# Kernel tuning notes

Measured on AMD Instinct MI355X. Metric: run time of the kernel, lower is better.

Reference implementation:

```python
import jax, jax.numpy as jnp
import numpy as np

DT = 0.01
EPS = 1e-5


def setup_inputs() -> dict:
    key = jax.random.key(0)
    ks = jax.random.split(key, 20)
    B, H, IN, COV, CH, OH, OUT = 1024, 64, 8, 16, 64, 128, 2
    NE, OPE = 400, 256            # events, observations per event
    TOT = NE * OPE

    def w(k, sh, sc=0.05):
        return jax.random.normal(k, sh, dtype=jnp.float32) * sc

    return {
        'time_uniq': jnp.arange(NE, dtype=jnp.float32) * DT,   # event k fires at grid step k
        'time_ptr': jnp.arange(NE + 1, dtype=jnp.int32) * OPE,  # uniform obs per event
        'X': jax.random.normal(ks[0], (TOT, IN), dtype=jnp.float32),
        'sample_ids': jax.random.randint(ks[1], (TOT,), 0, B, dtype=jnp.int32),
        'covs': jax.random.normal(ks[2], (B, COV), dtype=jnp.float32),
        'T': 5,
        'cov_W1': w(ks[3], (CH, COV)), 'cov_b1': jnp.zeros((CH,), jnp.float32),
        'cov_W2': w(ks[4], (H, CH)),   'cov_b2': jnp.zeros((H,), jnp.float32),
        'gb_Wih': w(ks[5], (3 * H, IN)), 'gb_Whh': w(ks[6], (3 * H, H)),
        'gb_bih': jnp.zeros((3 * H,), jnp.float32), 'gb_bhh': jnp.zeros((3 * H,), jnp.float32),
        'gx_W': w(ks[7], (3 * H, 1)), 'gx_b': jnp.zeros((3 * H,), jnp.float32),
        'ghr_W': w(ks[8], (H, H)), 'ghz_W': w(ks[9], (H, H)), 'ghh_W': w(ks[10], (H, H)),
        'out_W1': w(ks[11], (OH, H)), 'out_b1': jnp.zeros((OH,), jnp.float32),
        'out_W2': w(ks[12], (OUT, OH)), 'out_b2': jnp.zeros((OUT,), jnp.float32),
    }


def _forward(time_uniq, time_ptr, X, sample_ids, covs, T,
             cov_W1, cov_b1, cov_W2, cov_b2,
             gb_Wih, gb_Whh, gb_bih, gb_bhh,
             gx_W, gx_b, ghr_W, ghz_W, ghh_W,
             out_W1, out_b1, out_W2, out_b2):
    n_events = time_uniq.shape[0]
    ope = X.shape[0] // n_events          # uniform observations per event (static)
    n_steps = int(round(T / DT))
    delta_t = DT

    # covariates_map (dropout p=0 -> identity)
    h0 = jnp.tanh(jnp.maximum(covs @ cov_W1.T + cov_b1, 0.0) @ cov_W2.T + cov_b2)

    def gru_bayes(x, h):                  # torch.nn.GRUCell semantics (gates r,z,n)
        gi = x @ gb_Wih.T + gb_bih
        gh = h @ gb_Whh.T + gb_bhh
        ir, iz, inn = jnp.split(gi, 3, axis=1)
        hr, hz, hn = jnp.split(gh, 3, axis=1)
        r = jax.nn.sigmoid(ir + hr)
        z = jax.nn.sigmoid(iz + hz)
        n = jnp.tanh(inn + r * hn)
        return (1.0 - z) * n + z * h

    def gru_ode(h):                       # FullGRUODECell with x = zeros
        px = jnp.zeros((h.shape[0], 1), h.dtype)
        gx = px @ gx_W.T + gx_b
        xr, xz, xh = jnp.split(gx, 3, axis=1)
        r = jax.nn.sigmoid(xr + h @ ghr_W.T)
        z = jax.nn.sigmoid(xz + h @ ghz_W.T)
        u = jnp.tanh(xh + (r * h) @ ghh_W.T)
        return h + delta_t * (1.0 - z) * (u - h)

    times = jnp.arange(n_steps, dtype=jnp.float32) * DT
    offs = jnp.arange(ope)

    def step(carry, t):
        h, i = carry
        ic = jnp.minimum(i, n_events - 1)
        fire = (i < n_events) & (time_uniq[ic] <= t + EPS)   # <=1 event per grid step
        obs = time_ptr[ic] + offs
        idx = sample_ids[obs]
        h_upd = h.at[idx].set(gru_bayes(X[obs], h[idx]))
        h = jnp.where(fire, h_upd, h)
        i = i + fire.astype(i.dtype)
        h_rec = h                          # recorded after events, before ODE step
        h = gru_ode(h)
        return (h, i), h_rec

    (h_last, _), h_steps = jax.lax.scan(step, (h0, jnp.int32(0)), times)
    h_path = jnp.concatenate([h_steps, h_last[None]], axis=0)   # [n_steps+1, B, H]

    # net_out (dropout p=0 -> identity)
    o = jnp.maximum(jnp.einsum('tbh,oh->tbo', h_path, out_W1) + out_b1, 0.0)
    return jnp.einsum('tbh,oh->tbo', o, out_W2) + out_b2


def reference(time_uniq, time_ptr, X, sample_ids, covs, T,
              cov_W1, cov_b1, cov_W2, cov_b2,
              gb_Wih, gb_Whh, gb_bih, gb_bhh,
              gx_W, gx_b, ghr_W, ghz_W, ghh_W,
              out_W1, out_b1, out_W2, out_b2):
    return _forward(time_uniq, time_ptr, X, sample_ids, covs, T,
                    cov_W1, cov_b1, cov_W2, cov_b2,
                    gb_Wih, gb_Whh, gb_bih, gb_bhh,
                    gx_W, gx_b, ghr_W, ghz_W, ghh_W,
                    out_W1, out_b1, out_W2, out_b2)
```

## Files before the change

### kernel.cpp

```cpp
#include <hip/hip_runtime.h>

#define DT_F 0.01f
#define EPS_F 1e-5f
#define NEG_INF_I (-1073741824)

typedef _Float16 f16;
typedef _Float16 f16x2 __attribute__((ext_vector_type(2)));
typedef _Float16 f16x8 __attribute__((ext_vector_type(8)));
typedef float f32x4 __attribute__((ext_vector_type(4)));

#define MFMA16(a, b, c) __builtin_amdgcn_mfma_f32_16x16x32_f16((a), (b), (c), 0, 0, 0)

__device__ __forceinline__ float rl(float v, int l) {
  return __int_as_float(__builtin_amdgcn_readlane(__float_as_int(v), l));
}
__device__ __forceinline__ float sigm(float x) {
  float e = __builtin_amdgcn_exp2f(-1.442695041f * x);
  return __builtin_amdgcn_rcpf(1.0f + e);
}
__device__ __forceinline__ float tanhf_fast(float x) {
  float e = __builtin_amdgcn_exp2f(2.885390082f * x);
  return fmaf(-2.0f, __builtin_amdgcn_rcpf(e + 1.0f), 1.0f);
}
__device__ __forceinline__ float dot2(unsigned w, unsigned h, float acc) {
  return __builtin_amdgcn_fdot2(__builtin_bit_cast(f16x2, w),
                                __builtin_bit_cast(f16x2, h), acc, false);
}
__device__ __forceinline__ unsigned packf16(float a, float b) {
  return __builtin_bit_cast(unsigned, __builtin_amdgcn_cvt_pkrtz(a, b));
}
#define PINQ(v) asm volatile("" : "+v"((v).x), "+v"((v).y), "+v"((v).z), "+v"((v).w))

__global__ void build_evtab_kernel(const int* __restrict__ sample_ids,
                                   const int* __restrict__ time_ptr,
                                   int* __restrict__ evtab, int B, int ope) {
  int k = blockIdx.x;
  int base = time_ptr[k];
  for (int t = threadIdx.x; t < ope; t += blockDim.x) {
    int obs = base + t;
    int sid = sample_ids[obs];
    atomicMax(&evtab[k * B + sid], obs + 1);
  }
}

__global__ void pack_pairs_kernel(const float* __restrict__ ghr,
                                  const float* __restrict__ ghz,
                                  const float* __restrict__ ghh,
                                  const float* __restrict__ gbWhh,
                                  const float* __restrict__ gbWih,
                                  unsigned* __restrict__ odeP,
                                  unsigned* __restrict__ bayP,
                                  unsigned* __restrict__ wihP, int IN) {
  int idx = blockIdx.x * 256 + threadIdx.x;
  if (idx < 3 * 64 * 32) {
    int p = idx & 31, r = idx >> 5;
    int g = r >> 6, i = r & 63;
    const float* src = (g == 0) ? ghr : ((g == 1) ? ghz : ghh);
    odeP[idx] = packf16(src[i * 64 + 2 * p], src[i * 64 + 2 * p + 1]);
    bayP[idx] = packf16(gbWhh[r * 64 + 2 * p], gbWhh[r * 64 + 2 * p + 1]);
  }
  if (idx < 3 * 64 * 4) {
    int p = idx & 3, r = idx >> 2;
    float a = (2 * p < IN) ? gbWih[r * IN + 2 * p] : 0.0f;
    float b = (2 * p + 1 < IN) ? gbWih[r * IN + 2 * p + 1] : 0.0f;
    wihP[idx] = packf16(a, b);
  }
}

__global__ void pack_head_kernel(const float* __restrict__ W1, f16* __restrict__ w1P) {
  int f = blockIdx.x;
  int l = threadIdx.x;
  int t = f >> 1, kf = f & 1;
  int n = 16 * t + (l & 15);
  for (int j = 0; j < 8; ++j) {
    int k = 8 * (l >> 4) + j + 32 * kf;
    w1P[f * 512 + l * 8 + j] = (f16)W1[n * 64 + k];
  }
}

__global__ __launch_bounds__(256, 1) void evolve_kernel(
    const float* __restrict__ time_uniq,
    const float* __restrict__ X,
    const float* __restrict__ covs,
    const float* __restrict__ cov_W1, const float* __restrict__ cov_b1,
    const float* __restrict__ cov_W2, const float* __restrict__ cov_b2,
    const float* __restrict__ gb_bih, const float* __restrict__ gb_bhh,
    const float* __restrict__ gx_b,
    const unsigned* __restrict__ odeP, const unsigned* __restrict__ bayP,
    const unsigned* __restrict__ wihP,
    const int* __restrict__ evtab,
    f16* __restrict__ hp16,
    int B, int NE, int n_steps, int IN, int COV)
{
  __shared__ unsigned sBW[3 * 64 * 32];
  __shared__ int sStep[1024];
  __shared__ __align__(16) f16 sH16[4][64];
  __shared__ __align__(16) f16 sRH16[4][64];

  const int tid = threadIdx.x;
  const int wid = tid >> 6, lane = tid & 63;
  const int b = blockIdx.x * 4 + wid;
  const bool alive = (b < B);

  for (int idx = tid; idx < 3 * 64 * 32; idx += 256) {
    int c = idx & 31, r = idx >> 5;
    int i = r & 63, s = c >> 2;
    sBW[r * 32 + (((s ^ (i & 7)) << 2) | (c & 3))] = bayP[idx];
  }
  if (wid == 0) {
    int pm = NEG_INF_I;
    int loc[16];
#pragma unroll
    for (int j = 0; j < 16; ++j) {
      int e = lane * 16 + j;
      int gv = NEG_INF_I;
      if (e < NE && e < 1024) {
        float tu = time_uniq[e];
        int k0 = (int)floorf((tu - EPS_F) * 100.0f) - 2;
        if (k0 < 0) k0 = 0;
        while ((float)k0 * DT_F + EPS_F < tu) ++k0;
        gv = k0 - e;
      }
      pm = max(pm, gv);
      loc[j] = pm;
    }
    int tot = pm;
#pragma unroll
    for (int off = 1; off < 64; off <<= 1) {
      int v = __shfl_up(tot, off);
      if (lane >= off) tot = max(tot, v);
    }
    int excl = __shfl_up(tot, 1);
    if (lane == 0) excl = NEG_INF_I;
#pragma unroll
    for (int j = 0; j < 16; ++j)
      sStep[lane * 16 + j] = lane * 16 + j + max(loc[j], excl);
  }
  __syncthreads();

  const uint4* odeQ = (const uint4*)odeP;
  uint4 WR[8], WZ[8], WU[8];
#pragma unroll
  for (int q = 0; q < 8; ++q) {
    WR[q] = odeQ[(0 * 64 + lane) * 8 + q];
    WZ[q] = odeQ[(1 * 64 + lane) * 8 + q];
    WU[q] = odeQ[(2 * 64 + lane) * 8 + q];
  }
  const uint4* wihQ = (const uint4*)wihP;

  const float xr = gx_b[lane], xz = gx_b[64 + lane], xh = gx_b[128 + lane];
  const float crz_r = gb_bih[lane] + gb_bhh[lane];
  const float crz_z = gb_bih[64 + lane] + gb_bhh[64 + lane];
  const float bihn = gb_bih[128 + lane], bhhn = gb_bhh[128 + lane];

  float h = 0.0f;
  if (alive) {
    float cacc = cov_b1[lane];
    for (int c = 0; c < COV; ++c)
      cacc = fmaf(covs[b * COV + c], cov_W1[lane * COV + c], cacc);
    float cl = fmaxf(cacc, 0.0f);
    float hacc = cov_b2[lane];
#pragma unroll
    for (int j = 0; j < 64; ++j)
      hacc = fmaf(rl(cl, j), cov_W2[lane * 64 + j], hacc);
    h = tanhf_fast(hacc);
  }
  sH16[wid][lane] = (f16)h;

  int e_next = 0, s_next = 0x7fffffff, v_cur = 0, v_pipe = 0;
  float xf[8];
#pragma unroll
  for (int kk = 0; kk < 8; ++kk) xf[kk] = 0.0f;
  if (alive && NE > 0) {
    s_next = sStep[0];
    v_cur = evtab[b];
    if (v_cur > 0) {
      const float* xp = X + (long)(v_cur - 1) * IN;
#pragma unroll
      for (int kk = 0; kk < 8; ++kk) xf[kk] = (kk < IN) ? xp[kk] : 0.0f;
    }
    v_pipe = (NE > 1) ? evtab[B + b] : 0;
  } else if (NE > 0) {
    s_next = sStep[0];
  }

  const uint4* hq4 = (const uint4*)sH16[wid];
  const uint4* rq4 = (const uint4*)sRH16[wid];
  f16* hps = hp16 + (long)b * 64 + lane;
  const long rowstride = (long)B * 64;

  uint4 hpre[8];
#pragma unroll
  for (int q = 0; q < 8; ++q) hpre[q] = hq4[q];

#pragma unroll 1
  for (int k = 0; k < n_steps; ++k) {
#pragma unroll
    for (int q = 0; q < 8; ++q) { PINQ(WR[q]); PINQ(WZ[q]); PINQ(WU[q]); }

    if (k == s_next) {
      if (v_cur > 0) {
        unsigned xp0 = packf16(xf[0], xf[1]), xp1 = packf16(xf[2], xf[3]);
        unsigned xp2 = packf16(xf[4], xf[5]), xp3 = packf16(xf[6], xf[7]);
        uint4 wxr = wihQ[lane], wxz = wihQ[64 + lane], wxn = wihQ[128 + lane];
        float ar = crz_r, az = crz_z, anh = bhhn, ani = bihn;
        ar = dot2(wxr.x, xp0, ar); ar = dot2(wxr.y, xp1, ar);
        ar = dot2(wxr.z, xp2, ar); ar = dot2(wxr.w, xp3, ar);
        az = dot2(wxz.x, xp0, az); az = dot2(wxz.y, xp1, az);
        az = dot2(wxz.z, xp2, az); az = dot2(wxz.w, xp3, az);
        ani = dot2(wxn.x, xp0, ani); ani = dot2(wxn.y, xp1, ani);
        ani = dot2(wxn.z, xp2, ani); ani = dot2(wxn.w, xp3, ani);
        float ar1 = 0.f, az1 = 0.f, an1 = 0.f;
#pragma unroll
        for (int q = 0; q < 8; ++q) {
          uint4 hh = hpre[q];
          int sw = ((q ^ (lane & 7)) << 2);
          uint4 br = *(const uint4*)&sBW[(0 * 64 + lane) * 32 + sw];
          uint4 bz = *(const uint4*)&sBW[(1 * 64 + lane) * 32 + sw];
          uint4 bn = *(const uint4*)&sBW[(2 * 64 + lane) * 32 + sw];
          ar  = dot2(br.x, hh.x, ar);   ar1 = dot2(br.y, hh.y, ar1);
          ar  = dot2(br.z, hh.z, ar);   ar1 = dot2(br.w, hh.w, ar1);
          az  = dot2(bz.x, hh.x, az);   az1 = dot2(bz.y, hh.y, az1);
          az  = dot2(bz.z, hh.z, az);   az1 = dot2(bz.w, hh.w, az1);
          anh = dot2(bn.x, hh.x, anh);  an1 = dot2(bn.y, hh.y, an1);
          anh = dot2(bn.z, hh.z, anh);  an1 = dot2(bn.w, hh.w, an1);
        }
        float r = sigm(ar + ar1);
        float z = sigm(az + az1);
        float n = tanhf_fast(ani + r * (anh + an1));
        h = (1.0f - z) * n + z * h;
        sH16[wid][lane] = (f16)h;
#pragma unroll
        for (int q = 0; q < 8; ++q) hpre[q] = hq4[q];
      }
      ++e_next;
      if (e_next < NE && e_next < 1024) {
        s_next = sStep[e_next];
        v_cur = v_pipe;
        if (v_cur > 0) {
          const float* xp = X + (long)(v_cur - 1) * IN;
#pragma unroll
          for (int kk = 0; kk < 8; ++kk) xf[kk] = (kk < IN) ? xp[kk] : 0.0f;
        }
        v_pipe = (e_next + 1 < NE) ? evtab[(long)(e_next + 1) * B + b] : 0;
      } else {
        s_next = 0x7fffffff;
        v_cur = 0;
      }
    }

    if (alive)
      hps[(long)k * rowstride] = (f16)h;

    float ar0 = xr, ar1 = 0.f, ar2 = 0.f, ar3 = 0.f;
    float az0 = xz, az1 = 0.f, az2 = 0.f, az3 = 0.f;
#pragma unroll
    for (int q = 0; q < 8; ++q) {
      uint4 hp = hpre[q];
      ar0 = dot2(WR[q].x, hp.x, ar0); ar1 = dot2(WR[q].y, hp.y, ar1);
      ar2 = dot2(WR[q].z, hp.z, ar2); ar3 = dot2(WR[q].w, hp.w, ar3);
      az0 = dot2(WZ[q].x, hp.x, az0); az1 = dot2(WZ[q].y, hp.y, az1);
      az2 = dot2(WZ[q].z, hp.z, az2); az3 = dot2(WZ[q].w, hp.w, az3);
    }
    float r = sigm((ar0 + ar1) + (ar2 + ar3));
    float z = sigm((az0 + az1) + (az2 + az3));
    sRH16[wid][lane] = (f16)(r * h);

    float au0 = xh, au1 = 0.f, au2 = 0.f, au3 = 0.f;
#pragma unroll
    for (int q = 0; q < 8; ++q) {
      uint4 rp = rq4[q];
      au0 = dot2(WU[q].x, rp.x, au0); au1 = dot2(WU[q].y, rp.y, au1);
      au2 = dot2(WU[q].z, rp.z, au2); au3 = dot2(WU[q].w, rp.w, au3);
    }
    float u = tanhf_fast((au0 + au1) + (au2 + au3));
    h = fmaf(DT_F * (1.0f - z), u - h, h);
    sH16[wid][lane] = (f16)h;
#pragma unroll
    for (int q = 0; q < 8; ++q) hpre[q] = hq4[q];
  }

  if (alive)
    hps[(long)n_steps * rowstride] = (f16)h;
}

__global__ __launch_bounds__(256, 4) void head_mfma_kernel(
    const f16* __restrict__ hp16, const f16* __restrict__ w1P,
    const float* __restrict__ b1, const float* __restrict__ W2,
    const float* __restrict__ b2, float* __restrict__ out, long nrows)
{
  const int wq = threadIdx.x >> 6, lane = threadIdx.x & 63;
  const int col = lane & 15;
  const long rowbase = ((long)blockIdx.x * 4 + wq) * 64;

  f16x8 Wf[8][2];
#pragma unroll
  for (int t = 0; t < 8; ++t)
#pragma unroll
    for (int kf = 0; kf < 2; ++kf)
      Wf[t][kf] = ((const f16x8*)w1P)[(2 * t + kf) * 64 + lane];

  float b1v[8], w2a[8], w2b[8];
#pragma unroll
  for (int t = 0; t < 8; ++t) {
    b1v[t] = b1[16 * t + col];
    w2a[t] = W2[16 * t + col];
    w2b[t] = W2[128 + 16 * t + col];
  }
  const float b20 = b2[0], b21 = b2[1];

#pragma unroll 1
  for (int g = 0; g < 4; ++g) {
    long row0 = rowbase + g * 16;
    long arow = row0 + col;
    f16x8 aH0 = {0, 0, 0, 0, 0, 0, 0, 0}, aH1 = aH0;
    if (arow < nrows) {
      const f16x8* ap = (const f16x8*)(hp16 + arow * 64);
      aH0 = ap[lane >> 4];
      aH1 = ap[(lane >> 4) + 4];
    }
    float p0[4] = {0.f, 0.f, 0.f, 0.f}, p1[4] = {0.f, 0.f, 0.f, 0.f};
#pragma unroll
    for (int t = 0; t < 8; ++t) {
      f32x4 c = {0.f, 0.f, 0.f, 0.f};
      c = MFMA16(aH0, Wf[t][0], c);
      c = MFMA16(aH1, Wf[t][1], c);
#pragma unroll
      for (int i = 0; i < 4; ++i) {
        float o = fmaxf(c[i] + b1v[t], 0.0f);
        p0[i] = fmaf(o, w2a[t], p0[i]);
        p1[i] = fmaf(o, w2b[t], p1[i]);
      }
    }
#pragma unroll
    for (int off = 1; off < 16; off <<= 1) {
#pragma unroll
      for (int i = 0; i < 4; ++i) {
        p0[i] += __shfl_xor(p0[i], off);
        p1[i] += __shfl_xor(p1[i], off);
      }
    }
    if (col == 0) {
#pragma unroll
      for (int i = 0; i < 4; ++i) {
        long row = row0 + (lane >> 4) * 4 + i;
        if (row < nrows) {
          out[row * 2 + 0] = p0[i] + b20;
          out[row * 2 + 1] = p1[i] + b21;
        }
      }
    }
  }
}

extern "C" void kernel_launch(void* const* d_in, const int* in_sizes, int n_in,
                              void* d_out, int out_size, void* d_ws, size_t ws_size,
                              hipStream_t stream) {
  const float* time_uniq  = (const float*)d_in[0];
  const int*   time_ptr   = (const int*)d_in[1];
  const float* X          = (const float*)d_in[2];
  const int*   sample_ids = (const int*)d_in[3];
  const float* covs       = (const float*)d_in[4];
  const float* cov_W1     = (const float*)d_in[6];
  const float* cov_b1     = (const float*)d_in[7];
  const float* cov_W2     = (const float*)d_in[8];
  const float* cov_b2     = (const float*)d_in[9];
  const float* gb_Wih     = (const float*)d_in[10];
  const float* gb_Whh     = (const float*)d_in[11];
  const float* gb_bih     = (const float*)d_in[12];
  const float* gb_bhh     = (const float*)d_in[13];
  const float* gx_b       = (const float*)d_in[15];
  const float* ghr_W      = (const float*)d_in[16];
  const float* ghz_W      = (const float*)d_in[17];
  const float* ghh_W      = (const float*)d_in[18];
  const float* out_W1     = (const float*)d_in[19];
  const float* out_b1     = (const float*)d_in[20];
  const float* out_W2     = (const float*)d_in[21];
  const float* out_b2     = (const float*)d_in[22];

  int NE   = in_sizes[0];
  int TOT  = in_sizes[3];
  int IN   = in_sizes[2] / TOT;
  int CH   = in_sizes[7];
  int COV  = in_sizes[6] / CH;
  int B    = in_sizes[4] / COV;
  int OUTD = in_sizes[22];
  int n_steps = out_size / (B * OUTD) - 1;
  int OPE  = TOT / NE;

  char* ws = (char*)d_ws;
  int* evtab = (int*)ws;
  size_t evbytes = (size_t)NE * (size_t)B * sizeof(int);
  size_t off1 = (evbytes + 255) & ~(size_t)255;
  unsigned* odeP = (unsigned*)(ws + off1);
  unsigned* bayP = odeP + 3 * 64 * 32;
  unsigned* wihP = bayP + 3 * 64 * 32;
  size_t off2 = off1 + (((3 * 64 * 32 * 2 + 3 * 64 * 4) * sizeof(unsigned) + 255) & ~(size_t)255);
  f16* w1P = (f16*)(ws + off2);
  size_t off3 = off2 + ((16 * 512 * sizeof(f16) + 255) & ~(size_t)255);
  f16* hp16 = (f16*)(ws + off3);

  hipMemsetAsync(evtab, 0, evbytes, stream);
  build_evtab_kernel<<<NE, 256, 0, stream>>>(sample_ids, time_ptr, evtab, B, OPE);
  pack_pairs_kernel<<<24, 256, 0, stream>>>(ghr_W, ghz_W, ghh_W, gb_Whh, gb_Wih,
                                            odeP, bayP, wihP, IN);
  pack_head_kernel<<<16, 64, 0, stream>>>(out_W1, w1P);
  evolve_kernel<<<(B + 3) / 4, 256, 0, stream>>>(
      time_uniq, X, covs, cov_W1, cov_b1, cov_W2, cov_b2,
      gb_bih, gb_bhh, gx_b, odeP, bayP, wihP,
      evtab, hp16, B, NE, n_steps, IN, COV);
  long nrows = (long)(n_steps + 1) * B;
  int hb = (int)((nrows + 255) / 256);
  head_mfma_kernel<<<hb, 256, 0, stream>>>(hp16, w1P, out_b1, out_W2, out_b2,
                                           (float*)d_out, nrows);
}
```

Before: 453.8 us.

## Split each sample's ODE recurrence across two cooperating wavefronts

Each block now handles one sample with two wavefronts instead of four independent samples. Wave 1 computes the reset gate and r*h while wave 0 computes the update gate, candidate and event GRU update, with barriers handing data between them. The per-sample event table is staged into shared memory up front, so the step loop no longer makes scattered global reads for it. This shortens the per-step serial dependency chain at the cost of two or three block barriers per step and twice as many wavefronts in total.

```diff
diff --git a/kernel.cpp b/kernel.cpp
--- a/kernel.cpp
+++ b/kernel.cpp
@@ -29,7 +29,7 @@
 __device__ __forceinline__ unsigned packf16(float a, float b) {
   return __builtin_bit_cast(unsigned, __builtin_amdgcn_cvt_pkrtz(a, b));
 }
-#define PINQ(v) asm volatile("" : "+v"((v).x), "+v"((v).y), "+v"((v).z), "+v"((v).w))
+#define ANCH4(v) asm volatile("" : "+v"((v).x), "+v"((v).y), "+v"((v).z), "+v"((v).w))
 
 __global__ void build_evtab_kernel(const int* __restrict__ sample_ids,
                                    const int* __restrict__ time_ptr,
@@ -78,7 +78,7 @@
   }
 }
 
-__global__ __launch_bounds__(256, 1) void evolve_kernel(
+__global__ __launch_bounds__(128, 2) void evolve_kernel(
     const float* __restrict__ time_uniq,
     const float* __restrict__ X,
     const float* __restrict__ covs,
@@ -94,19 +94,22 @@
 {
   __shared__ unsigned sBW[3 * 64 * 32];
   __shared__ int sStep[1024];
-  __shared__ __align__(16) f16 sH16[4][64];
-  __shared__ __align__(16) f16 sRH16[4][64];
+  __shared__ int sEvt[1024];
+  __shared__ __align__(16) f16 sHimg[64];
+  __shared__ __align__(16) f16 sRHimg[64];
 
   const int tid = threadIdx.x;
   const int wid = tid >> 6, lane = tid & 63;
-  const int b = blockIdx.x * 4 + wid;
-  const bool alive = (b < B);
-
-  for (int idx = tid; idx < 3 * 64 * 32; idx += 256) {
+  const int b = blockIdx.x;
+  const int necap = (NE < 1024) ? NE : 1024;
+
+  for (int idx = tid; idx < 3 * 64 * 32; idx += 128) {
     int c = idx & 31, r = idx >> 5;
     int i = r & 63, s = c >> 2;
     sBW[r * 32 + (((s ^ (i & 7)) << 2) | (c & 3))] = bayP[idx];
   }
+  for (int e = tid; e < necap; e += 128)
+    sEvt[e] = evtab[(long)e * B + b];
   if (wid == 0) {
     int pm = NEG_INF_I;
     int loc[16];
@@ -114,7 +117,7 @@
     for (int j = 0; j < 16; ++j) {
       int e = lane * 16 + j;
       int gv = NEG_INF_I;
-      if (e < NE && e < 1024) {
+      if (e < necap) {
         float tu = time_uniq[e];
         int k0 = (int)floorf((tu - EPS_F) * 100.0f) - 2;
         if (k0 < 0) k0 = 0;
@@ -136,25 +139,7 @@
     for (int j = 0; j < 16; ++j)
       sStep[lane * 16 + j] = lane * 16 + j + max(loc[j], excl);
   }
-  __syncthreads();
-
-  const uint4* odeQ = (const uint4*)odeP;
-  uint4 WR[8], WZ[8], WU[8];
-#pragma unroll
-  for (int q = 0; q < 8; ++q) {
-    WR[q] = odeQ[(0 * 64 + lane) * 8 + q];
-    WZ[q] = odeQ[(1 * 64 + lane) * 8 + q];
-    WU[q] = odeQ[(2 * 64 + lane) * 8 + q];
-  }
-  const uint4* wihQ = (const uint4*)wihP;
-
-  const float xr = gx_b[lane], xz = gx_b[64 + lane], xh = gx_b[128 + lane];
-  const float crz_r = gb_bih[lane] + gb_bhh[lane];
-  const float crz_z = gb_bih[64 + lane] + gb_bhh[64 + lane];
-  const float bihn = gb_bih[128 + lane], bhhn = gb_bhh[128 + lane];
-
-  float h = 0.0f;
-  if (alive) {
+  if (wid == 0) {
     float cacc = cov_b1[lane];
     for (int c = 0; c < COV; ++c)
       cacc = fmaf(covs[b * COV + c], cov_W1[lane * COV + c], cacc);
@@ -163,125 +148,172 @@
 #pragma unroll
     for (int j = 0; j < 64; ++j)
       hacc = fmaf(rl(cl, j), cov_W2[lane * 64 + j], hacc);
-    h = tanhf_fast(hacc);
-  }
-  sH16[wid][lane] = (f16)h;
-
-  int e_next = 0, s_next = 0x7fffffff, v_cur = 0, v_pipe = 0;
-  float xf[8];
-#pragma unroll
-  for (int kk = 0; kk < 8; ++kk) xf[kk] = 0.0f;
-  if (alive && NE > 0) {
-    s_next = sStep[0];
-    v_cur = evtab[b];
-    if (v_cur > 0) {
-      const float* xp = X + (long)(v_cur - 1) * IN;
-#pragma unroll
-      for (int kk = 0; kk < 8; ++kk) xf[kk] = (kk < IN) ? xp[kk] : 0.0f;
-    }
-    v_pipe = (NE > 1) ? evtab[B + b] : 0;
-  } else if (NE > 0) {
-    s_next = sStep[0];
-  }
-
-  const uint4* hq4 = (const uint4*)sH16[wid];
-  const uint4* rq4 = (const uint4*)sRH16[wid];
-  f16* hps = hp16 + (long)b * 64 + lane;
-  const long rowstride = (long)B * 64;
-
-  uint4 hpre[8];
-#pragma unroll
-  for (int q = 0; q < 8; ++q) hpre[q] = hq4[q];
+    sHimg[lane] = (f16)tanhf_fast(hacc);
+  }
+  __syncthreads();
+
+  const uint4* odeQ = (const uint4*)odeP;
+  const uint4* hq4 = (const uint4*)sHimg;
+  const uint4* rq4 = (const uint4*)sRHimg;
+
+  if (wid == 0) {
+    uint4 WZ[8], WU[8];
+#pragma unroll
+    for (int q = 0; q < 8; ++q) {
+      WZ[q] = odeQ[(1 * 64 + lane) * 8 + q];
+      WU[q] = odeQ[(2 * 64 + lane) * 8 + q];
+    }
+#pragma unroll
+    for (int q = 0; q < 8; ++q) { ANCH4(WZ[q]); ANCH4(WU[q]); }
+    const uint4* wihQ = (const uint4*)wihP;
+
+    const float xz = gx_b[64 + lane], xh = gx_b[128 + lane];
+    const float crz_r = gb_bih[lane] + gb_bhh[lane];
+    const float crz_z = gb_bih[64 + lane] + gb_bhh[64 + lane];
+    const float bihn = gb_bih[128 + lane], bhhn = gb_bhh[128 + lane];
+
+    float h = (float)sHimg[lane];
+    f16* hps = hp16 + (long)b * 64 + lane;
+    const long rowstride = (long)B * 64;
+
+    int e_next = 0, s_next = 0x7fffffff, v_cur = 0, v_pipe = 0;
+    float xf[8];
+#pragma unroll
+    for (int kk = 0; kk < 8; ++kk) xf[kk] = 0.0f;
+    if (necap > 0) {
+      s_next = sStep[0];
+      v_cur = sEvt[0];
+      if (v_cur > 0) {
+        const float* xp = X + (long)(v_cur - 1) * IN;
+#pragma unroll
+        for (int kk = 0; kk < 8; ++kk) xf[kk] = (kk < IN) ? xp[kk] : 0.0f;
+      }
+      v_pipe = (necap > 1) ? sEvt[1] : 0;
+    }
 
 #pragma unroll 1
-  for (int k = 0; k < n_steps; ++k) {
-#pragma unroll
-    for (int q = 0; q < 8; ++q) { PINQ(WR[q]); PINQ(WZ[q]); PINQ(WU[q]); }
-
-    if (k == s_next) {
-      if (v_cur > 0) {
-        unsigned xp0 = packf16(xf[0], xf[1]), xp1 = packf16(xf[2], xf[3]);
-        unsigned xp2 = packf16(xf[4], xf[5]), xp3 = packf16(xf[6], xf[7]);
-        uint4 wxr = wihQ[lane], wxz = wihQ[64 + lane], wxn = wihQ[128 + lane];
-        float ar = crz_r, az = crz_z, anh = bhhn, ani = bihn;
-        ar = dot2(wxr.x, xp0, ar); ar = dot2(wxr.y, xp1, ar);
-        ar = dot2(wxr.z, xp2, ar); ar = dot2(wxr.w, xp3, ar);
-        az = dot2(wxz.x, xp0, az); az = dot2(wxz.y, xp1, az);
-        az = dot2(wxz.z, xp2, az); az = dot2(wxz.w, xp3, az);
-        ani = dot2(wxn.x, xp0, ani); ani = dot2(wxn.y, xp1, ani);
-        ani = dot2(wxn.z, xp2, ani); ani = dot2(wxn.w, xp3, ani);
-        float ar1 = 0.f, az1 = 0.f, an1 = 0.f;
-#pragma unroll
-        for (int q = 0; q < 8; ++q) {
-          uint4 hh = hpre[q];
-          int sw = ((q ^ (lane & 7)) << 2);
-          uint4 br = *(const uint4*)&sBW[(0 * 64 + lane) * 32 + sw];
-          uint4 bz = *(const uint4*)&sBW[(1 * 64 + lane) * 32 + sw];
-          uint4 bn = *(const uint4*)&sBW[(2 * 64 + lane) * 32 + sw];
-          ar  = dot2(br.x, hh.x, ar);   ar1 = dot2(br.y, hh.y, ar1);
-          ar  = dot2(br.z, hh.z, ar);   ar1 = dot2(br.w, hh.w, ar1);
-          az  = dot2(bz.x, hh.x, az);   az1 = dot2(bz.y, hh.y, az1);
-          az  = dot2(bz.z, hh.z, az);   az1 = dot2(bz.w, hh.w, az1);
-          anh = dot2(bn.x, hh.x, anh);  an1 = dot2(bn.y, hh.y, an1);
-          anh = dot2(bn.z, hh.z, anh);  an1 = dot2(bn.w, hh.w, an1);
+    for (int k = 0; k < n_steps; ++k) {
+      if (k == s_next) {
+        const bool fire = (v_cur > 0);
+        if (fire) {
+          unsigned xp0 = packf16(xf[0], xf[1]), xp1 = packf16(xf[2], xf[3]);
+          unsigned xp2 = packf16(xf[4], xf[5]), xp3 = packf16(xf[6], xf[7]);
+          uint4 wxr = wihQ[lane], wxz = wihQ[64 + lane], wxn = wihQ[128 + lane];
+          float ar = crz_r, az = crz_z, anh = bhhn, ani = bihn;
+          ar = dot2(wxr.x, xp0, ar); ar = dot2(wxr.y, xp1, ar);
+          ar = dot2(wxr.z, xp2, ar); ar = dot2(wxr.w, xp3, ar);
+          az = dot2(wxz.x, xp0, az); az = dot2(wxz.y, xp1, az);
+          az = dot2(wxz.z, xp2, az); az = dot2(wxz.w, xp3, az);
+          ani = dot2(wxn.x, xp0, ani); ani = dot2(wxn.y, xp1, ani);
+          ani = dot2(wxn.z, xp2, ani); ani = dot2(wxn.w, xp3, ani);
+          float ar1 = 0.f, az1 = 0.f, an1 = 0.f;
+#pragma unroll
+          for (int q = 0; q < 8; ++q) {
+            uint4 hh = hq4[q];
+            int sw = ((q ^ (lane & 7)) << 2);
+            uint4 br = *(const uint4*)&sBW[(0 * 64 + lane) * 32 + sw];
+            uint4 bz = *(const uint4*)&sBW[(1 * 64 + lane) * 32 + sw];
+            uint4 bn = *(const uint4*)&sBW[(2 * 64 + lane) * 32 + sw];
+            ar  = dot2(br.x, hh.x, ar);   ar1 = dot2(br.y, hh.y, ar1);
+            ar  = dot2(br.z, hh.z, ar);   ar1 = dot2(br.w, hh.w, ar1);
+            az  = dot2(bz.x, hh.x, az);   az1 = dot2(bz.y, hh.y, az1);
+            az  = dot2(bz.z, hh.z, az);   az1 = dot2(bz.w, hh.w, az1);
+            anh = dot2(bn.x, hh.x, anh);  an1 = dot2(bn.y, hh.y, an1);
+            anh = dot2(bn.z, hh.z, anh);  an1 = dot2(bn.w, hh.w, an1);
+          }
+          float r = sigm(ar + ar1);
+          float z = sigm(az + az1);
+          float n = tanhf_fast(ani + r * (anh + an1));
+          h = (1.0f - z) * n + z * h;
+          sHimg[lane] = (f16)h;
         }
-        float r = sigm(ar + ar1);
-        float z = sigm(az + az1);
-        float n = tanhf_fast(ani + r * (anh + an1));
-        h = (1.0f - z) * n + z * h;
-        sH16[wid][lane] = (f16)h;
-#pragma unroll
-        for (int q = 0; q < 8; ++q) hpre[q] = hq4[q];
-      }
-      ++e_next;
-      if (e_next < NE && e_next < 1024) {
-        s_next = sStep[e_next];
-        v_cur = v_pipe;
-        if (v_cur > 0) {
-          const float* xp = X + (long)(v_cur - 1) * IN;
-#pragma unroll
-          for (int kk = 0; kk < 8; ++kk) xf[kk] = (kk < IN) ? xp[kk] : 0.0f;
+        ++e_next;
+        if (e_next < necap) {
+          s_next = sStep[e_next];
+          v_cur = v_pipe;
+          if (v_cur > 0) {
+            const float* xp = X + (long)(v_cur - 1) * IN;
+#pragma unroll
+            for (int kk = 0; kk < 8; ++kk) xf[kk] = (kk < IN) ? xp[kk] : 0.0f;
+          }
+          v_pipe = (e_next + 1 < necap) ? sEvt[e_next + 1] : 0;
+        } else {
+          s_next = 0x7fffffff;
+          v_cur = 0;
         }
-        v_pipe = (e_next + 1 < NE) ? evtab[(long)(e_next + 1) * B + b] : 0;
-      } else {
-        s_next = 0x7fffffff;
-        v_cur = 0;
-      }
-    }
-
-    if (alive)
+        if (fire) __syncthreads();
+      }
+
       hps[(long)k * rowstride] = (f16)h;
 
-    float ar0 = xr, ar1 = 0.f, ar2 = 0.f, ar3 = 0.f;
-    float az0 = xz, az1 = 0.f, az2 = 0.f, az3 = 0.f;
-#pragma unroll
-    for (int q = 0; q < 8; ++q) {
-      uint4 hp = hpre[q];
-      ar0 = dot2(WR[q].x, hp.x, ar0); ar1 = dot2(WR[q].y, hp.y, ar1);
-      ar2 = dot2(WR[q].z, hp.z, ar2); ar3 = dot2(WR[q].w, hp.w, ar3);
-      az0 = dot2(WZ[q].x, hp.x, az0); az1 = dot2(WZ[q].y, hp.y, az1);
-      az2 = dot2(WZ[q].z, hp.z, az2); az3 = dot2(WZ[q].w, hp.w, az3);
-    }
-    float r = sigm((ar0 + ar1) + (ar2 + ar3));
-    float z = sigm((az0 + az1) + (az2 + az3));
-    sRH16[wid][lane] = (f16)(r * h);
-
-    float au0 = xh, au1 = 0.f, au2 = 0.f, au3 = 0.f;
-#pragma unroll
-    for (int q = 0; q < 8; ++q) {
-      uint4 rp = rq4[q];
-      au0 = dot2(WU[q].x, rp.x, au0); au1 = dot2(WU[q].y, rp.y, au1);
-      au2 = dot2(WU[q].z, rp.z, au2); au3 = dot2(WU[q].w, rp.w, au3);
-    }
-    float u = tanhf_fast((au0 + au1) + (au2 + au3));
-    h = fmaf(DT_F * (1.0f - z), u - h, h);
-    sH16[wid][lane] = (f16)h;
-#pragma unroll
-    for (int q = 0; q < 8; ++q) hpre[q] = hq4[q];
-  }
-
-  if (alive)
+      float az0 = xz, az1 = 0.f, az2 = 0.f, az3 = 0.f;
+#pragma unroll
+      for (int q = 0; q < 8; ++q) {
+        uint4 hp = hq4[q];
+        az0 = dot2(WZ[q].x, hp.x, az0); az1 = dot2(WZ[q].y, hp.y, az1);
+        az2 = dot2(WZ[q].z, hp.z, az2); az3 = dot2(WZ[q].w, hp.w, az3);
+      }
+      float z = sigm((az0 + az1) + (az2 + az3));
+      __syncthreads();
+
+      float au0 = xh, au1 = 0.f, au2 = 0.f, au3 = 0.f;
+#pragma unroll
+      for (int q = 0; q < 8; ++q) {
+        uint4 rp = rq4[q];
+        au0 = dot2(WU[q].x, rp.x, au0); au1 = dot2(WU[q].y, rp.y, au1);
+        au2 = dot2(WU[q].z, rp.z, au2); au3 = dot2(WU[q].w, rp.w, au3);
+      }
+      float u = tanhf_fast((au0 + au1) + (au2 + au3));
+      h = fmaf(DT_F * (1.0f - z), u - h, h);
+      sHimg[lane] = (f16)h;
+      __syncthreads();
+    }
     hps[(long)n_steps * rowstride] = (f16)h;
+  } else {
+    uint4 WR[8];
+#pragma unroll
+    for (int q = 0; q < 8; ++q) WR[q] = odeQ[(0 * 64 + lane) * 8 + q];
+#pragma unroll
+    for (int q = 0; q < 8; ++q) ANCH4(WR[q]);
+    const float xr = gx_b[lane];
+
+    int e_next = 0, s_next = 0x7fffffff, v_cur = 0, v_pipe = 0;
+    if (necap > 0) {
+      s_next = sStep[0];
+      v_cur = sEvt[0];
+      v_pipe = (necap > 1) ? sEvt[1] : 0;
+    }
+
+#pragma unroll 1
+    for (int k = 0; k < n_steps; ++k) {
+      if (k == s_next) {
+        const bool fire = (v_cur > 0);
+        ++e_next;
+        if (e_next < necap) {
+          s_next = sStep[e_next];
+          v_cur = v_pipe;
+          v_pipe = (e_next + 1 < necap) ? sEvt[e_next + 1] : 0;
+        } else {
+          s_next = 0x7fffffff;
+          v_cur = 0;
+        }
+        if (fire) __syncthreads();
+      }
+
+      float ar0 = xr, ar1 = 0.f, ar2 = 0.f, ar3 = 0.f;
+#pragma unroll
+      for (int q = 0; q < 8; ++q) {
+        uint4 hp = hq4[q];
+        ar0 = dot2(WR[q].x, hp.x, ar0); ar1 = dot2(WR[q].y, hp.y, ar1);
+        ar2 = dot2(WR[q].z, hp.z, ar2); ar3 = dot2(WR[q].w, hp.w, ar3);
+      }
+      float r = sigm((ar0 + ar1) + (ar2 + ar3));
+      float hf = (float)sHimg[lane];
+      sRHimg[lane] = (f16)(r * hf);
+      __syncthreads();
+      __syncthreads();
+    }
+  }
 }
 
 __global__ __launch_bounds__(256, 4) void head_mfma_kernel(
@@ -405,7 +437,7 @@
   pack_pairs_kernel<<<24, 256, 0, stream>>>(ghr_W, ghz_W, ghh_W, gb_Whh, gb_Wih,
                                             odeP, bayP, wihP, IN);
   pack_head_kernel<<<16, 64, 0, stream>>>(out_W1, w1P);
-  evolve_kernel<<<(B + 3) / 4, 256, 0, stream>>>(
+  evolve_kernel<<<B, 128, 0, stream>>>(
       time_uniq, X, covs, cov_W1, cov_b1, cov_W2, cov_b2,
       gb_bih, gb_bhh, gx_b, odeP, bayP, wihP,
       evtab, hp16, B, NE, n_steps, IN, COV);
```

Result: faster. 433.3 us (-4.5%).
